# Performance work log

Measured on AMD Instinct MI355X. Metric: run time of the kernel, lower is better.

Reference implementation:

```python
import jax, jax.numpy as jnp
from jax import lax
import numpy as np

B, L, E, K, NCLS = 128, 1024, 8, 3, 5


def conv1d(x, w, b):
    # x: [N,C,L], w: [O,I,3], padding=1 -> same length
    y = lax.conv_general_dilated(x, w, (1,), [(1, 1)], dimension_numbers=('NCH', 'OIH', 'NCH'))
    return y + b[None, :, None]


def maxpool2(x):
    # MaxPool1d(kernel=2, stride=2), floor mode (VALID drops odd tail)
    return lax.reduce_window(x, -jnp.inf, lax.max, (1, 1, 2), (1, 1, 2), 'VALID')


def setup_inputs():
    key = jax.random.key(0)
    ks = jax.random.split(key, 32)
    s = 0.05
    g = lambda i, shp: jax.random.normal(ks[i], shp, jnp.float32) * s
    inp = {}
    inp['x'] = jax.random.normal(ks[0], (B, 1, L), jnp.float32)
    inp['c1_w'], inp['c1_b'] = g(1, (16, 1, 3)), jnp.zeros((16,), jnp.float32)
    # stacked expert conv params (leading dim = E)
    chans = [(16, 16), (16, 32), (32, 64), (64, 128), (128, 256), (256, 512)]
    for j, (ci, co) in enumerate(chans, start=1):
        inp[f'ew{j}'] = g(1 + j, (E, co, ci, 3))
        inp[f'eb{j}'] = jnp.zeros((E, co), jnp.float32)
    inp['r_w'], inp['r_b'] = g(10, (E, 16)), jnp.zeros((E,), jnp.float32)
    inp['c2_w'], inp['c2_b'] = g(11, (1024, 512, 3)), jnp.zeros((1024,), jnp.float32)
    fl = (L // 8 // 2) * 1024
    inp['f1_w'], inp['f1_b'] = g(12, (256, fl)) * 0.2, jnp.zeros((256,), jnp.float32)
    inp['f2_w'], inp['f2_b'] = g(13, (NCLS, 256)), jnp.zeros((NCLS,), jnp.float32)
    return inp


def reference(x, c1_w, c1_b, ew1, eb1, ew2, eb2, ew3, eb3, ew4, eb4, ew5, eb5, ew6, eb6,
              r_w, r_b, c2_w, c2_b, f1_w, f1_b, f2_w, f2_b):
    b = x.shape[0]
    h = jax.nn.relu(conv1d(x, c1_w, c1_b))            # [B,16,L]
    pooled = h.mean(axis=-1)                           # AdaptiveAvgPool1d(1) -> [B,16]
    # (router noise skipped: eval-mode determinism)
    rlogits = pooled @ r_w.T + r_b                     # [B,E]
    probs = jax.nn.softmax(rlogits, axis=-1)
    tg, ti = lax.top_k(probs, K)                       # [B,K]
    tg = tg / tg.sum(axis=-1, keepdims=True)
    gates = jnp.zeros((b, E), probs.dtype).at[jnp.arange(b)[:, None], ti].set(tg)  # dense [B,E]

    def expert(w1, b1, w2, b2, w3, b3, w4, b4, w5, b5, w6, b6):
        y = conv1d(h, w1, b1)
        y = maxpool2(jax.nn.relu(conv1d(y, w2, b2)))   # block1 -> [B,32,L/2]
        y = conv1d(y, w3, b3)
        y = maxpool2(jax.nn.relu(conv1d(y, w4, b4)))   # block2 -> [B,128,L/4]
        y = conv1d(y, w5, b5)
        y = maxpool2(jax.nn.relu(conv1d(y, w6, b6)))   # block3 -> [B,512,L/8]
        return y

    eouts = jax.vmap(expert)(ew1, eb1, ew2, eb2, ew3, eb3, ew4, eb4, ew5, eb5, ew6, eb6)  # [E,B,512,L/8]
    combined = jnp.einsum('be,ebcl->bcl', gates, eouts)  # gated scatter-combine (zero gate == not dispatched)

    y = maxpool2(jax.nn.relu(conv1d(combined, c2_w, c2_b)))  # [B,1024,L/16]
    y = y.reshape(b, -1)
    y = jax.nn.relu(y @ f1_w.T + f1_b)                 # dropout p=0.05 is identity in eval
    out = y @ f2_w.T + f2_b                            # [B,NCLS]

    mean_probs = probs.mean(axis=0)
    cv = jnp.std(mean_probs, ddof=1) / (mean_probs.mean() + 1e-10)  # torch std is unbiased
    return out, cv ** 2
```

## Files before the change

kernel.cpp:

```cpp
#include <hip/hip_runtime.h>
#include <hip/hip_bf16.h>
#include <math.h>

#define B_   128
#define L_   1024
#define E_   8
#define K_   3

typedef float f32x4 __attribute__((ext_vector_type(4)));
typedef short s8v  __attribute__((ext_vector_type(8)));
typedef unsigned short u16x8 __attribute__((ext_vector_type(8)));

__device__ inline ushort f2bf(float v) {
  union { float f; unsigned u; } x; x.f = v;
  unsigned r = (x.u + 0x7fffu + ((x.u >> 16) & 1u)) >> 16;
  return (ushort)r;
}
__device__ inline float bf2f(ushort h) {
  union { unsigned u; float f; } x; x.u = ((unsigned)h) << 16;
  return x.f;
}

__device__ __forceinline__ void gload_lds16(const ushort* g, ushort* l) {
  __builtin_amdgcn_global_load_lds(
      (const __attribute__((address_space(1))) unsigned int*)g,
      (__attribute__((address_space(3))) unsigned int*)l, 16, 0, 0);
}

__global__ __launch_bounds__(256) void conv1_k(
    const float* __restrict__ x, const float* __restrict__ w,
    const float* __restrict__ bias, float* __restrict__ h,
    float* __restrict__ pooled)
{
  const int b = blockIdx.x;
  const int t = threadIdx.x;
  __shared__ float xs[1026];
  __shared__ float wsm[48];
  __shared__ float bs[16];
  __shared__ float red[4][16];

  for (int i = t; i < 1024; i += 256) xs[i + 1] = x[(size_t)b * 1024 + i];
  if (t == 0) { xs[0] = 0.f; xs[1025] = 0.f; }
  if (t < 48) wsm[t] = w[t];
  if (t < 16) bs[t] = bias[t];
  __syncthreads();

  float ps[16];
#pragma unroll
  for (int c = 0; c < 16; ++c) ps[c] = 0.f;

  for (int li = 0; li < 4; ++li) {
    const int l = t + li * 256;
    const float xm = xs[l], x0 = xs[l + 1], xp = xs[l + 2];
#pragma unroll
    for (int co = 0; co < 16; ++co) {
      float v = fmaf(wsm[co * 3 + 0], xm,
                fmaf(wsm[co * 3 + 1], x0,
                fmaf(wsm[co * 3 + 2], xp, bs[co])));
      v = fmaxf(v, 0.f);
      h[((size_t)b * 16 + co) * 1024 + l] = v;
      ps[co] += v;
    }
  }
#pragma unroll
  for (int co = 0; co < 16; ++co) {
    float v = ps[co];
    for (int off = 32; off > 0; off >>= 1) v += __shfl_down(v, off, 64);
    ps[co] = v;
  }
  const int wid = t >> 6, lane = t & 63;
  if (lane == 0) {
#pragma unroll
    for (int co = 0; co < 16; ++co) red[wid][co] = ps[co];
  }
  __syncthreads();
  if (t < 16) pooled[(size_t)b * 16 + t] =
      (red[0][t] + red[1][t] + red[2][t] + red[3][t]) * (1.f / 1024.f);
}

__global__ void router_k(const float* __restrict__ pooled,
                         const float* __restrict__ rw,
                         const float* __restrict__ rb,
                         float* __restrict__ pair_g, int* __restrict__ pair_e,
                         float* __restrict__ cv2_out)
{
  const int b = threadIdx.x;
  __shared__ float pl[128][8];
  __shared__ float mp[8];

  float pv[16];
#pragma unroll
  for (int i = 0; i < 16; ++i) pv[i] = pooled[(size_t)b * 16 + i];

  float lg[8];
#pragma unroll
  for (int e = 0; e < 8; ++e) {
    float s = rb[e];
#pragma unroll
    for (int i = 0; i < 16; ++i) s = fmaf(pv[i], rw[e * 16 + i], s);
    lg[e] = s;
  }
  float mx = lg[0];
#pragma unroll
  for (int e = 1; e < 8; ++e) mx = fmaxf(mx, lg[e]);
  float pr[8]; float sum = 0.f;
#pragma unroll
  for (int e = 0; e < 8; ++e) { pr[e] = expf(lg[e] - mx); sum += pr[e]; }
  const float inv = 1.f / sum;
#pragma unroll
  for (int e = 0; e < 8; ++e) { pr[e] *= inv; pl[b][e] = pr[e]; }

  bool used[8] = {false,false,false,false,false,false,false,false};
  float tg[3]; int ti[3];
  for (int k = 0; k < 3; ++k) {
    float best = -1.f; int bi = 0;
#pragma unroll
    for (int e = 0; e < 8; ++e)
      if (!used[e] && pr[e] > best) { best = pr[e]; bi = e; }
    used[bi] = true; tg[k] = best; ti[k] = bi;
  }
  const float ts = 1.f / (tg[0] + tg[1] + tg[2]);
  for (int k = 0; k < 3; ++k) {
    pair_g[b * 3 + k] = tg[k] * ts;
    pair_e[b * 3 + k] = ti[k];
  }
  __syncthreads();
  if (b < 8) {
    float s = 0.f;
    for (int i = 0; i < 128; ++i) s += pl[i][b];
    mp[b] = s * (1.f / 128.f);
  }
  __syncthreads();
  if (b == 0) {
    float m = 0.f;
    for (int e = 0; e < 8; ++e) m += mp[e];
    m *= (1.f / 8.f);
    float v = 0.f;
    for (int e = 0; e < 8; ++e) { float d = mp[e] - m; v += d * d; }
    v *= (1.f / 7.f);
    const float cv = sqrtf(v) / (m + 1e-10f);
    cv2_out[0] = cv * cv;
  }
}

template <int CI, int CO, int LIN, bool POOL, int CIC, int CO_T, int CO_R,
          int IN_DIV>
__global__ __launch_bounds__(256) void convR_k(
    const float* __restrict__ in, const float* __restrict__ w,
    const float* __restrict__ bias, float* __restrict__ out,
    const int* __restrict__ pe)
{
  constexpr int CQ  = CO_T / CO_R;
  constexpr int LQ  = 256 / CQ;
  constexpr int L_T = LQ * 4;
  constexpr int LOUT = POOL ? (LIN / 2) : LIN;
  constexpr int RS  = L_T + 8;
  constexpr int CG  = CO_R / 4;

  const int p  = blockIdx.x;
  const int cb = blockIdx.y * CO_T;
  const int l0 = blockIdx.z * L_T;
  const int e  = pe ? pe[p] : 0;
  const float* inp = in + (size_t)(p / IN_DIV) * CI * LIN;
  const float* wp  = w + (size_t)e * CO * CI * 3;

  __shared__ float in_s[CIC * RS];
  __shared__ float w_s[CIC * 3 * CO_T];

  const int t  = threadIdx.x;
  const int cq = t / LQ;
  const int lq = t % LQ;

  float acc[CO_R][4];
#pragma unroll
  for (int c = 0; c < CO_R; ++c)
#pragma unroll
    for (int l = 0; l < 4; ++l) acc[c][l] = 0.f;

  for (int c0 = 0; c0 < CI; c0 += CIC) {
    for (int idx = t; idx < CIC * (L_T + 2); idx += 256) {
      const int ci = idx / (L_T + 2);
      const int j  = idx - ci * (L_T + 2);
      const int gl = l0 + j - 1;
      in_s[ci * RS + j] =
          (gl >= 0 && gl < LIN) ? inp[(size_t)(c0 + ci) * LIN + gl] : 0.f;
    }
    for (int i = t; i < CIC * CO_T; i += 256) {
      const int co = i % CO_T;
      const int ci = i / CO_T;
      const float* wsrc = wp + ((size_t)(cb + co) * CI + (c0 + ci)) * 3;
      const float w0 = wsrc[0], w1 = wsrc[1], w2 = wsrc[2];
      w_s[(ci * 3 + 0) * CO_T + co] = w0;
      w_s[(ci * 3 + 1) * CO_T + co] = w1;
      w_s[(ci * 3 + 2) * CO_T + co] = w2;
    }
    __syncthreads();
#pragma unroll 4
    for (int ci = 0; ci < CIC; ++ci) {
      const float* row = &in_s[ci * RS + lq * 4];
      const float4 xa = *reinterpret_cast<const float4*>(row);
      const float2 xb = *reinterpret_cast<const float2*>(row + 4);
      const float xv[6] = {xa.x, xa.y, xa.z, xa.w, xb.x, xb.y};
      const float* wrow = &w_s[ci * 3 * CO_T + cq * CO_R];
#pragma unroll
      for (int k = 0; k < 3; ++k) {
#pragma unroll
        for (int cg = 0; cg < CG; ++cg) {
          const float4 wv =
              *reinterpret_cast<const float4*>(&wrow[k * CO_T + cg * 4]);
          const float wq[4] = {wv.x, wv.y, wv.z, wv.w};
#pragma unroll
          for (int c = 0; c < 4; ++c)
#pragma unroll
            for (int l = 0; l < 4; ++l)
              acc[cg * 4 + c][l] = fmaf(wq[c], xv[l + k], acc[cg * 4 + c][l]);
        }
      }
    }
    __syncthreads();
  }

#pragma unroll
  for (int c = 0; c < CO_R; ++c) {
    const int co = cb + cq * CO_R + c;
    const float bv = bias[(size_t)e * CO + co];
    const float v0 = acc[c][0] + bv, v1 = acc[c][1] + bv;
    const float v2 = acc[c][2] + bv, v3 = acc[c][3] + bv;
    float* op = out + ((size_t)p * CO + co) * LOUT;
    if (POOL) {
      const int lo = (l0 >> 1) + lq * 2;
      float2 r;
      r.x = fmaxf(fmaxf(v0, v1), 0.f);
      r.y = fmaxf(fmaxf(v2, v3), 0.f);
      *reinterpret_cast<float2*>(&op[lo]) = r;
    } else {
      const int l = l0 + lq * 4;
      *reinterpret_cast<float4*>(&op[l]) = make_float4(v0, v1, v2, v3);
    }
  }
}

struct WSeg { const float* w; ushort* oh; ushort* ol; int CO; int CI; int n; };

__global__ void wprepAll_k(const float* w3, const float* w4,
                           const float* w5, const float* w6,
                           const float* wF,
                           ushort* o3h, ushort* o3l, ushort* o4h, ushort* o4l,
                           ushort* o5h, ushort* o5l, ushort* o6h, ushort* o6l,
                           ushort* oFh, ushort* oFl)
{
  int idx = blockIdx.x * 256 + threadIdx.x;
  const float* w; ushort* oh; ushort* ol; int CO, CI;
  if (idx < 49152)        { w = w3; oh = o3h; ol = o3l; CO = 64;   CI = 32;  }
  else if (idx < 245760)  { idx -= 49152;
                            w = w4; oh = o4h; ol = o4l; CO = 128;  CI = 64;  }
  else if (idx < 1032192) { idx -= 245760;
                            w = w5; oh = o5h; ol = o5l; CO = 256;  CI = 128; }
  else if (idx < 4177920) { idx -= 1032192;
                            w = w6; oh = o6h; ol = o6l; CO = 512;  CI = 256; }
  else if (idx < 5750784) { idx -= 4177920;
                            w = wF; oh = oFh; ol = oFl; CO = 1024; CI = 512; }
  else return;

  const int KC = CI >> 5;
  const int j = idx & 31;
  int r = idx >> 5;
  const int co = r % CO; r /= CO;
  const int kc = r % KC; r /= KC;
  const int tp = r % 3;
  const int e  = r / 3;
  const float v = w[(((size_t)e * CO + co) * CI + (kc * 32 + j)) * 3 + tp];
  const ushort hi = f2bf(v);
  oh[idx] = hi;
  ol[idx] = f2bf(v - bf2f(hi));
}

__global__ __launch_bounds__(256) void t0_k(const float* __restrict__ in,
                                            ushort* __restrict__ oh,
                                            ushort* __restrict__ ol)
{
  __shared__ float tile[32][33];
  const int p  = blockIdx.x;
  const int l0 = blockIdx.y * 32;
  const int tx = threadIdx.x & 31;
  const int ty = threadIdx.x >> 5;

#pragma unroll
  for (int i = 0; i < 4; ++i) {
    const int ci = ty + i * 8;
    tile[ci][tx] = in[(size_t)p * 16384 + (size_t)ci * 512 + l0 + tx];
  }
  __syncthreads();
#pragma unroll
  for (int i = 0; i < 4; ++i) {
    const int l = l0 + ty + i * 8;
    const float v = tile[tx][ty + i * 8];
    const size_t o = ((size_t)p * 514 + 1 + l) * 32 + tx;
    const ushort hi = f2bf(v);
    oh[o] = hi;
    ol[o] = f2bf(v - bf2f(hi));
  }
  if (blockIdx.y == 0 && threadIdx.x < 32) {
    const size_t o0 = (size_t)p * 514 * 32 + threadIdx.x;
    const size_t o1 = ((size_t)p * 514 + 513) * 32 + threadIdx.x;
    oh[o0] = 0; ol[o0] = 0; oh[o1] = 0; ol[o1] = 0;
  }
}

template <int CI, int CO, int L, int OMODE>
__global__ __launch_bounds__(256) void convM_k(
    const ushort* __restrict__ xh, const ushort* __restrict__ xl,
    const ushort* __restrict__ wh, const ushort* __restrict__ wl,
    const float* __restrict__ bias,
    ushort* __restrict__ oh, ushort* __restrict__ ol,
    float* __restrict__ of,
    const int* __restrict__ pe, const float* __restrict__ pg,
    int pair0)
{
  constexpr int KC = CI / 32;
  constexpr int NK = (OMODE == 1) ? 3 : 1;
  const int bx = blockIdx.x;
  const int cb = blockIdx.y * 64;
  const int lz = blockIdx.z * 128;

  __shared__ ushort xs[2][130][32];
  __shared__ ushort wsm[2][3][64][32];
  ushort* xsf = &xs[0][0][0];
  ushort* wsf = &wsm[0][0][0][0];

  const int t = threadIdx.x;
  const int lane = t & 63;
  const int wv = t >> 6;
  const int l16 = lane & 15;
  const int kb8 = (lane >> 4) * 8;

  float gacc[2][4][2];
  if (OMODE == 1) {
#pragma unroll
    for (int a = 0; a < 2; ++a)
#pragma unroll
      for (int b = 0; b < 4; ++b) { gacc[a][b][0] = 0.f; gacc[a][b][1] = 0.f; }
  }

  f32x4 acc[2][4];
  int e = 0; float gate = 1.f; int lp = bx;
  float bv[4];

  for (int kp = 0; kp < NK; ++kp) {
    if (OMODE == 1) {
      const int gp = (pair0 + bx) * 3 + kp;
      e = pe[gp]; gate = pg[gp]; lp = bx * 3 + kp;
    } else if (OMODE == 2) { lp = bx; e = 0; }
    else { lp = bx; e = pe[pair0 + bx]; }

#pragma unroll
    for (int a = 0; a < 2; ++a)
#pragma unroll
      for (int b = 0; b < 4; ++b) acc[a][b] = (f32x4){0.f, 0.f, 0.f, 0.f};

    const size_t xbase = ((size_t)lp * (L + 2) + lz) * CI;

    for (int kc = 0; kc < KC; ++kc) {
      const int c0 = kc * 32;
#pragma unroll
      for (int it = 0; it < 5; ++it) {
        const int g = it * 256 + t;
        if (g < 1040) {
          const int pl = g >= 520;
          const int r = g - pl * 520;
          const int row = r >> 2;
          const int c16 = r & 3;
          const ushort* src =
              (pl ? xl : xh) + xbase + (size_t)row * CI + c0 + c16 * 8;
          gload_lds16(src, xsf + (size_t)g * 8);
        }
      }
#pragma unroll
      for (int it = 0; it < 6; ++it) {
        const int g = it * 256 + t;
        const int pl = g >= 768;
        const int r = g - pl * 768;
        const int tp = r >> 8;
        const int rr = r & 255;
        const int co = rr >> 2;
        const int c16 = rr & 3;
        const ushort* src = (pl ? wl : wh) +
            ((((size_t)e * 3 + tp) * KC + kc) * CO + cb + co) * 32 + c16 * 8;
        gload_lds16(src, wsf + (size_t)g * 8);
      }
      __syncthreads();

      __builtin_amdgcn_s_setprio(1);
#pragma unroll
      for (int tp = 0; tp < 3; ++tp) {
        const int ar = wv * 32 + l16 + tp;
        s8v a00 = *reinterpret_cast<const s8v*>(&xs[0][ar][kb8]);
        s8v a01 = *reinterpret_cast<const s8v*>(&xs[0][ar + 16][kb8]);
        s8v a10 = *reinterpret_cast<const s8v*>(&xs[1][ar][kb8]);
        s8v a11 = *reinterpret_cast<const s8v*>(&xs[1][ar + 16][kb8]);
#pragma unroll
        for (int cs = 0; cs < 4; ++cs) {
          const int brow = cs * 16 + l16;
          s8v bh = *reinterpret_cast<const s8v*>(&wsm[0][tp][brow][kb8]);
          s8v bl = *reinterpret_cast<const s8v*>(&wsm[1][tp][brow][kb8]);
          acc[0][cs] = __builtin_amdgcn_mfma_f32_16x16x32_bf16(a00, bh, acc[0][cs], 0, 0, 0);
          acc[0][cs] = __builtin_amdgcn_mfma_f32_16x16x32_bf16(a00, bl, acc[0][cs], 0, 0, 0);
          acc[0][cs] = __builtin_amdgcn_mfma_f32_16x16x32_bf16(a10, bh, acc[0][cs], 0, 0, 0);
          acc[1][cs] = __builtin_amdgcn_mfma_f32_16x16x32_bf16(a01, bh, acc[1][cs], 0, 0, 0);
          acc[1][cs] = __builtin_amdgcn_mfma_f32_16x16x32_bf16(a01, bl, acc[1][cs], 0, 0, 0);
          acc[1][cs] = __builtin_amdgcn_mfma_f32_16x16x32_bf16(a11, bh, acc[1][cs], 0, 0, 0);
        }
      }
      __builtin_amdgcn_s_setprio(0);
      __syncthreads();
    }

#pragma unroll
    for (int cs = 0; cs < 4; ++cs)
      bv[cs] = bias[(size_t)e * CO + cb + cs * 16 + l16];

    if (OMODE == 1) {
#pragma unroll
      for (int ls = 0; ls < 2; ++ls)
#pragma unroll
        for (int cs = 0; cs < 4; ++cs)
#pragma unroll
          for (int q = 0; q < 2; ++q) {
            const float v0 = acc[ls][cs][q * 2] + bv[cs];
            const float v1 = acc[ls][cs][q * 2 + 1] + bv[cs];
            const float m = fmaxf(fmaxf(v0, v1), 0.f);
            gacc[ls][cs][q] += gate * m;
          }
    }
  }

  if (OMODE == 0) {
#pragma unroll
    for (int ls = 0; ls < 2; ++ls)
#pragma unroll
      for (int cs = 0; cs < 4; ++cs)
#pragma unroll
        for (int r = 0; r < 4; ++r) {
          const int l = lz + wv * 32 + ls * 16 + (lane >> 4) * 4 + r;
          const float v = acc[ls][cs][r] + bv[cs];
          const size_t o = ((size_t)lp * (L + 2) + 1 + l) * CO + cb + cs * 16 + l16;
          const ushort hi = f2bf(v);
          oh[o] = hi;
          ol[o] = f2bf(v - bf2f(hi));
        }
    if (blockIdx.z == 0 && t < 64) {
      const size_t o0 = (size_t)lp * (L + 2) * CO + cb + t;
      const size_t o1 = ((size_t)lp * (L + 2) + (L + 1)) * CO + cb + t;
      oh[o0] = 0; ol[o0] = 0; oh[o1] = 0; ol[o1] = 0;
    }
  } else if (OMODE == 3) {
#pragma unroll
    for (int ls = 0; ls < 2; ++ls)
#pragma unroll
      for (int cs = 0; cs < 4; ++cs)
#pragma unroll
        for (int r = 0; r < 4; r += 2) {
          const float v0 = acc[ls][cs][r] + bv[cs];
          const float v1 = acc[ls][cs][r + 1] + bv[cs];
          const float m = fmaxf(fmaxf(v0, v1), 0.f);
          const int lpp = (lz + wv * 32 + ls * 16 + (lane >> 4) * 4 + r) >> 1;
          const size_t o = ((size_t)lp * (L / 2 + 2) + 1 + lpp) * CO + cb + cs * 16 + l16;
          const ushort hi = f2bf(m);
          oh[o] = hi;
          ol[o] = f2bf(m - bf2f(hi));
        }
    if (blockIdx.z == 0 && t < 64) {
      const size_t o0 = (size_t)lp * (L / 2 + 2) * CO + cb + t;
      const size_t o1 = ((size_t)lp * (L / 2 + 2) + (L / 2 + 1)) * CO + cb + t;
      oh[o0] = 0; ol[o0] = 0; oh[o1] = 0; ol[o1] = 0;
    }
  } else if (OMODE == 1) {
#pragma unroll
    for (int ls = 0; ls < 2; ++ls)
#pragma unroll
      for (int cs = 0; cs < 4; ++cs)
#pragma unroll
        for (int q = 0; q < 2; ++q) {
          const int lpp = (lz + wv * 32 + ls * 16 + (lane >> 4) * 4 + q * 2) >> 1;
          const int co = cb + cs * 16 + l16;
          const size_t o =
              ((size_t)(pair0 + bx) * (L / 2 + 2) + 1 + lpp) * CO + co;
          const float g = gacc[ls][cs][q];
          const ushort hi = f2bf(g);
          oh[o] = hi;
          ol[o] = f2bf(g - bf2f(hi));
        }
    if (blockIdx.z == 0 && t < 64) {
      const size_t o0 = (size_t)(pair0 + bx) * (L / 2 + 2) * CO + cb + t;
      const size_t o1 =
          ((size_t)(pair0 + bx) * (L / 2 + 2) + (L / 2 + 1)) * CO + cb + t;
      oh[o0] = 0; ol[o0] = 0; oh[o1] = 0; ol[o1] = 0;
    }
  } else {
#pragma unroll
    for (int ls = 0; ls < 2; ++ls)
#pragma unroll
      for (int cs = 0; cs < 4; ++cs)
#pragma unroll
        for (int r = 0; r < 4; r += 2) {
          const float v0 = acc[ls][cs][r] + bv[cs];
          const float v1 = acc[ls][cs][r + 1] + bv[cs];
          const float m = fmaxf(fmaxf(v0, v1), 0.f);
          const int lpp = (lz + wv * 32 + ls * 16 + (lane >> 4) * 4 + r) >> 1;
          const int co = cb + cs * 16 + l16;
          const size_t o = ((size_t)lp * CO + co) * (L / 2) + lpp;
          of[o] = m;
        }
  }
}

__global__ __launch_bounds__(256) void fc1M_k(const float* __restrict__ X,
                                              const float* __restrict__ W,
                                              float* __restrict__ part)
{
  __shared__ ushort xs[2][128][32];
  __shared__ ushort wsm[2][64][32];
  const int t = threadIdx.x;
  const int lane = t & 63;
  const int wv = t >> 6;
  const int l16 = lane & 15;
  const int kb8 = (lane >> 4) * 8;
  const int ot = blockIdx.x * 64;
  const size_t k0g = (size_t)blockIdx.y * 512;

  f32x4 acc[2][4];
#pragma unroll
  for (int a = 0; a < 2; ++a)
#pragma unroll
    for (int b = 0; b < 4; ++b) acc[a][b] = (f32x4){0.f, 0.f, 0.f, 0.f};

  const int xrow = t >> 1;
  const int xcol = (t & 1) * 16;
  const int wco  = t >> 2;
  const int wk   = (t & 3) * 8;

  for (int it = 0; it < 16; ++it) {
    const size_t k0 = k0g + it * 32;
    {
      const float* src = X + (size_t)xrow * 65536 + k0 + xcol;
      float v[16];
#pragma unroll
      for (int q = 0; q < 4; ++q)
        *reinterpret_cast<float4*>(&v[q * 4]) =
            *reinterpret_cast<const float4*>(src + q * 4);
#pragma unroll
      for (int q = 0; q < 2; ++q) {
        u16x8 hv, lv;
#pragma unroll
        for (int j = 0; j < 8; ++j) {
          const float f = v[q * 8 + j];
          const ushort h = f2bf(f);
          hv[j] = h;
          lv[j] = f2bf(f - bf2f(h));
        }
        *reinterpret_cast<u16x8*>(&xs[0][xrow][xcol + q * 8]) = hv;
        *reinterpret_cast<u16x8*>(&xs[1][xrow][xcol + q * 8]) = lv;
      }
    }
    {
      const float* src = W + (size_t)(ot + wco) * 65536 + k0 + wk;
      float v[8];
      *reinterpret_cast<float4*>(&v[0]) = *reinterpret_cast<const float4*>(src);
      *reinterpret_cast<float4*>(&v[4]) = *reinterpret_cast<const float4*>(src + 4);
      u16x8 hv, lv;
#pragma unroll
      for (int j = 0; j < 8; ++j) {
        const ushort h = f2bf(v[j]);
        hv[j] = h;
        lv[j] = f2bf(v[j] - bf2f(h));
      }
      *reinterpret_cast<u16x8*>(&wsm[0][wco][wk]) = hv;
      *reinterpret_cast<u16x8*>(&wsm[1][wco][wk]) = lv;
    }
    __syncthreads();
    __builtin_amdgcn_s_setprio(1);
#pragma unroll
    for (int ms = 0; ms < 2; ++ms) {
      const int ar = wv * 32 + ms * 16 + l16;
      s8v ah = *reinterpret_cast<const s8v*>(&xs[0][ar][kb8]);
      s8v al = *reinterpret_cast<const s8v*>(&xs[1][ar][kb8]);
#pragma unroll
      for (int cs = 0; cs < 4; ++cs) {
        const int brow = cs * 16 + l16;
        s8v bh = *reinterpret_cast<const s8v*>(&wsm[0][brow][kb8]);
        s8v bl = *reinterpret_cast<const s8v*>(&wsm[1][brow][kb8]);
        acc[ms][cs] = __builtin_amdgcn_mfma_f32_16x16x32_bf16(ah, bh, acc[ms][cs], 0, 0, 0);
        acc[ms][cs] = __builtin_amdgcn_mfma_f32_16x16x32_bf16(ah, bl, acc[ms][cs], 0, 0, 0);
        acc[ms][cs] = __builtin_amdgcn_mfma_f32_16x16x32_bf16(al, bh, acc[ms][cs], 0, 0, 0);
      }
    }
    __builtin_amdgcn_s_setprio(0);
    __syncthreads();
  }

#pragma unroll
  for (int ms = 0; ms < 2; ++ms)
#pragma unroll
    for (int cs = 0; cs < 4; ++cs)
#pragma unroll
      for (int r = 0; r < 4; ++r) {
        const int row = wv * 32 + ms * 16 + (lane >> 4) * 4 + r;
        const int col = ot + cs * 16 + l16;
        part[((size_t)blockIdx.y * 128 + row) * 256 + col] = acc[ms][cs][r];
      }
}

__global__ void fc1red_k(const float* __restrict__ part,
                         const float* __restrict__ b1, float* __restrict__ o1)
{
  const int idx = blockIdx.x * 256 + threadIdx.x;
  if (idx < 32768) {
    float s = 0.f;
#pragma unroll 8
    for (int z = 0; z < 128; ++z) s += part[(size_t)z * 32768 + idx];
    o1[idx] = fmaxf(s + b1[idx & 255], 0.f);
  }
}

__global__ void fc2_k(const float* __restrict__ o1, const float* __restrict__ w2,
                      const float* __restrict__ b2, float* __restrict__ out)
{
  const int b = blockIdx.x;
  const int lane = threadIdx.x;
  float acc[5] = {0.f, 0.f, 0.f, 0.f, 0.f};
  for (int i = lane; i < 256; i += 64) {
    const float xv = o1[(size_t)b * 256 + i];
#pragma unroll
    for (int o = 0; o < 5; ++o) acc[o] = fmaf(xv, w2[o * 256 + i], acc[o]);
  }
#pragma unroll
  for (int o = 0; o < 5; ++o) {
    for (int off = 32; off > 0; off >>= 1)
      acc[o] += __shfl_down(acc[o], off, 64);
  }
  if (lane == 0) {
#pragma unroll
    for (int o = 0; o < 5; ++o) out[b * 5 + o] = acc[o] + b2[o];
  }
}

extern "C" void kernel_launch(void* const* d_in, const int* in_sizes, int n_in,
                              void* d_out, int out_size, void* d_ws,
                              size_t ws_size, hipStream_t stream)
{
  const float* x   = (const float*)d_in[0];
  const float* c1w = (const float*)d_in[1];
  const float* c1b = (const float*)d_in[2];
  const float* ew[6];
  const float* eb[6];
  for (int j = 0; j < 6; ++j) {
    ew[j] = (const float*)d_in[3 + 2 * j];
    eb[j] = (const float*)d_in[4 + 2 * j];
  }
  const float* rw  = (const float*)d_in[15];
  const float* rb  = (const float*)d_in[16];
  const float* c2w = (const float*)d_in[17];
  const float* c2b = (const float*)d_in[18];
  const float* f1w = (const float*)d_in[19];
  const float* f1b = (const float*)d_in[20];
  const float* f2w = (const float*)d_in[21];
  const float* f2b = (const float*)d_in[22];
  float* out = (float*)d_out;

  const int chunkB = 32;
  const int chunkP = chunkB * 3;
  const int nchunk = 128 / chunkB;

  char* basep = (char*)d_ws;
  size_t off = 0;
  auto alloc = [&](size_t bytes) -> void* {
    off = (off + 255) & ~(size_t)255;
    void* r = basep + off;
    off += bytes;
    return r;
  };

  float* h      = (float*)alloc(2097152ull * 4);
  float* pooled = (float*)alloc(2048ull * 4);
  float* pairg  = (float*)alloc(384ull * 4);
  int*   paire  = (int*)  alloc(384ull * 4);
  float* fc1o   = (float*)alloc(32768ull * 4);

  ushort* xtFh  = (ushort*)alloc(8519680ull * 2 * 2);
  ushort* xtFl  = xtFh + 8519680ull;
  float*  part  = (float*)xtFh;

  const size_t slot_base = (off + 255) & ~(size_t)255;
  char* slotA = (char*)alloc((size_t)chunkP * 33024 * 2 * 2);
  char* slotB = (char*)alloc((size_t)chunkP * 66048 * 2 * 2);
  float* comb = (float*)(basep + slot_base);

  float*  bufA  = (float*)slotA;
  ushort* xt3h  = (ushort*)slotA;
  ushort* xt3l  = xt3h + (size_t)chunkP * 16448;
  ushort* xt5h  = (ushort*)slotA;
  ushort* xt5l  = xt5h + (size_t)chunkP * 33024;
  float*  bufB  = (float*)slotB;
  ushort* yE3h  = (ushort*)slotB;
  ushort* yE3l  = yE3h + (size_t)chunkP * 32896;
  ushort* y5h   = (ushort*)slotB;
  ushort* y5l   = y5h + (size_t)chunkP * 66048;

  ushort* wp3h  = (ushort*)alloc(49152ull * 2);
  ushort* wp3l  = (ushort*)alloc(49152ull * 2);
  ushort* wp4h  = (ushort*)alloc(196608ull * 2);
  ushort* wp4l  = (ushort*)alloc(196608ull * 2);
  ushort* wp5h  = (ushort*)alloc(786432ull * 2);
  ushort* wp5l  = (ushort*)alloc(786432ull * 2);
  ushort* wp6h  = (ushort*)alloc(3145728ull * 2);
  ushort* wp6l  = (ushort*)alloc(3145728ull * 2);
  ushort* wpFh  = (ushort*)alloc(1572864ull * 2);
  ushort* wpFl  = (ushort*)alloc(1572864ull * 2);

  conv1_k<<<128, 256, 0, stream>>>(x, c1w, c1b, h, pooled);
  router_k<<<1, 128, 0, stream>>>(pooled, rw, rb, pairg, paire, out + 640);

  wprepAll_k<<<(5750784 + 255) / 256, 256, 0, stream>>>(
      ew[2], ew[3], ew[4], ew[5], c2w,
      wp3h, wp3l, wp4h, wp4l, wp5h, wp5l, wp6h, wp6l, wpFh, wpFl);

  for (int c = 0; c < nchunk; ++c) {
    const int b0 = c * chunkB;
    const int p0 = c * chunkP;
    convR_k<16, 16, 1024, false, 16, 16, 4, 3>
        <<<dim3(chunkP, 1, 4), 256, 0, stream>>>(
            h + (size_t)b0 * 16 * 1024, ew[0], eb[0], bufA, paire + p0);
    convR_k<16, 32, 1024, true, 16, 32, 8, 1>
        <<<dim3(chunkP, 1, 4), 256, 0, stream>>>(bufA, ew[1], eb[1], bufB,
                                                 paire + p0);
    t0_k<<<dim3(chunkP, 16), 256, 0, stream>>>(bufB, xt3h, xt3l);
    convM_k<32, 64, 512, 0>
        <<<dim3(chunkP, 1, 4), 256, 0, stream>>>(xt3h, xt3l, wp3h, wp3l, eb[2],
                                                 yE3h, yE3l, nullptr, paire,
                                                 nullptr, p0);
    convM_k<64, 128, 512, 3>
        <<<dim3(chunkP, 2, 4), 256, 0, stream>>>(yE3h, yE3l, wp4h, wp4l, eb[3],
                                                 xt5h, xt5l, nullptr, paire,
                                                 nullptr, p0);
    convM_k<128, 256, 256, 0>
        <<<dim3(chunkP, 4, 2), 256, 0, stream>>>(xt5h, xt5l, wp5h, wp5l, eb[4],
                                                 y5h, y5l, nullptr, paire,
                                                 nullptr, p0);
    convM_k<256, 512, 256, 1>
        <<<dim3(chunkB, 8, 2), 256, 0, stream>>>(y5h, y5l, wp6h, wp6l, eb[5],
                                                 xtFh, xtFl, nullptr,
                                                 paire, pairg, b0);
  }

  convM_k<512, 1024, 128, 2>
      <<<dim3(128, 16, 1), 256, 0, stream>>>(xtFh, xtFl, wpFh, wpFl, c2b,
                                             nullptr, nullptr, comb, nullptr,
                                             nullptr, 0);

  fc1M_k<<<dim3(4, 128), 256, 0, stream>>>(comb, f1w, part);
  fc1red_k<<<128, 256, 0, stream>>>(part, f1b, fc1o);
  fc2_k<<<128, 64, 0, stream>>>(fc1o, f2w, f2b, out);
}
```

Baseline: 643.2 us.

## Fuse transpose/bf16 split into conv2 epilogue and enlarge batch chunk

The second expert conv kernel now writes its pooled output directly in the transposed, padded bf16 hi/lo layout that the MFMA conv consumes, which removes the separate t0_k transpose kernel and its fp32 round trip through memory. The xt3 buffer gets its own allocation because it can no longer alias slotA. The batch chunk size also grows to 64 when the workspace is large enough, halving the number of per-chunk launches at the cost of more workspace. The fused stores are strided scalar ushort writes (stride CO), which may coalesce worse than the old tiled transpose.

```diff
diff --git a/kernel.cpp b/kernel.cpp
--- a/kernel.cpp
+++ b/kernel.cpp
@@ -144,10 +144,11 @@
 }
 
 template <int CI, int CO, int LIN, bool POOL, int CIC, int CO_T, int CO_R,
-          int IN_DIV>
+          int IN_DIV, bool TPOSE>
 __global__ __launch_bounds__(256) void convR_k(
     const float* __restrict__ in, const float* __restrict__ w,
     const float* __restrict__ bias, float* __restrict__ out,
+    ushort* __restrict__ oh, ushort* __restrict__ ol,
     const int* __restrict__ pe)
 {
   constexpr int CQ  = CO_T / CO_R;
@@ -226,21 +227,39 @@
     const float bv = bias[(size_t)e * CO + co];
     const float v0 = acc[c][0] + bv, v1 = acc[c][1] + bv;
     const float v2 = acc[c][2] + bv, v3 = acc[c][3] + bv;
-    float* op = out + ((size_t)p * CO + co) * LOUT;
-    if (POOL) {
+    if (TPOSE) {
+      const float m0 = fmaxf(fmaxf(v0, v1), 0.f);
+      const float m1 = fmaxf(fmaxf(v2, v3), 0.f);
       const int lo = (l0 >> 1) + lq * 2;
-      float2 r;
-      r.x = fmaxf(fmaxf(v0, v1), 0.f);
-      r.y = fmaxf(fmaxf(v2, v3), 0.f);
-      *reinterpret_cast<float2*>(&op[lo]) = r;
+      const size_t o0 = ((size_t)p * (LIN / 2 + 2) + 1 + lo) * CO + co;
+      const ushort h0 = f2bf(m0);
+      oh[o0] = h0;
+      ol[o0] = f2bf(m0 - bf2f(h0));
+      const ushort h1 = f2bf(m1);
+      oh[o0 + CO] = h1;
+      ol[o0 + CO] = f2bf(m1 - bf2f(h1));
     } else {
-      const int l = l0 + lq * 4;
-      *reinterpret_cast<float4*>(&op[l]) = make_float4(v0, v1, v2, v3);
-    }
-  }
-}
-
-struct WSeg { const float* w; ushort* oh; ushort* ol; int CO; int CI; int n; };
+      float* op = out + ((size_t)p * CO + co) * LOUT;
+      if (POOL) {
+        const int lo = (l0 >> 1) + lq * 2;
+        float2 r;
+        r.x = fmaxf(fmaxf(v0, v1), 0.f);
+        r.y = fmaxf(fmaxf(v2, v3), 0.f);
+        *reinterpret_cast<float2*>(&op[lo]) = r;
+      } else {
+        const int l = l0 + lq * 4;
+        *reinterpret_cast<float4*>(&op[l]) = make_float4(v0, v1, v2, v3);
+      }
+    }
+  }
+  if (TPOSE) {
+    if (blockIdx.z == 0 && t < CO) {
+      const size_t o0 = (size_t)p * (LIN / 2 + 2) * CO + t;
+      const size_t o1 = ((size_t)p * (LIN / 2 + 2) + (LIN / 2 + 1)) * CO + t;
+      oh[o0] = 0; ol[o0] = 0; oh[o1] = 0; ol[o1] = 0;
+    }
+  }
+}
 
 __global__ void wprepAll_k(const float* w3, const float* w4,
                            const float* w5, const float* w6,
@@ -273,38 +292,6 @@
   const ushort hi = f2bf(v);
   oh[idx] = hi;
   ol[idx] = f2bf(v - bf2f(hi));
-}
-
-__global__ __launch_bounds__(256) void t0_k(const float* __restrict__ in,
-                                            ushort* __restrict__ oh,
-                                            ushort* __restrict__ ol)
-{
-  __shared__ float tile[32][33];
-  const int p  = blockIdx.x;
-  const int l0 = blockIdx.y * 32;
-  const int tx = threadIdx.x & 31;
-  const int ty = threadIdx.x >> 5;
-
-#pragma unroll
-  for (int i = 0; i < 4; ++i) {
-    const int ci = ty + i * 8;
-    tile[ci][tx] = in[(size_t)p * 16384 + (size_t)ci * 512 + l0 + tx];
-  }
-  __syncthreads();
-#pragma unroll
-  for (int i = 0; i < 4; ++i) {
-    const int l = l0 + ty + i * 8;
-    const float v = tile[tx][ty + i * 8];
-    const size_t o = ((size_t)p * 514 + 1 + l) * 32 + tx;
-    const ushort hi = f2bf(v);
-    oh[o] = hi;
-    ol[o] = f2bf(v - bf2f(hi));
-  }
-  if (blockIdx.y == 0 && threadIdx.x < 32) {
-    const size_t o0 = (size_t)p * 514 * 32 + threadIdx.x;
-    const size_t o1 = ((size_t)p * 514 + 513) * 32 + threadIdx.x;
-    oh[o0] = 0; ol[o0] = 0; oh[o1] = 0; ol[o1] = 0;
-  }
 }
 
 template <int CI, int CO, int L, int OMODE>
@@ -667,7 +654,7 @@
   const float* f2b = (const float*)d_in[22];
   float* out = (float*)d_out;
 
-  const int chunkB = 32;
+  const int chunkB = (ws_size >= 160000000ull) ? 64 : 32;
   const int chunkP = chunkB * 3;
   const int nchunk = 128 / chunkB;
 
@@ -691,20 +678,20 @@
   float*  part  = (float*)xtFh;
 
   const size_t slot_base = (off + 255) & ~(size_t)255;
-  char* slotA = (char*)alloc((size_t)chunkP * 33024 * 2 * 2);
-  char* slotB = (char*)alloc((size_t)chunkP * 66048 * 2 * 2);
+  char* slotA = (char*)alloc((size_t)chunkP * 132096);
+  char* slotB = (char*)alloc((size_t)chunkP * 264192);
   float* comb = (float*)(basep + slot_base);
 
   float*  bufA  = (float*)slotA;
-  ushort* xt3h  = (ushort*)slotA;
-  ushort* xt3l  = xt3h + (size_t)chunkP * 16448;
   ushort* xt5h  = (ushort*)slotA;
   ushort* xt5l  = xt5h + (size_t)chunkP * 33024;
-  float*  bufB  = (float*)slotB;
   ushort* yE3h  = (ushort*)slotB;
   ushort* yE3l  = yE3h + (size_t)chunkP * 32896;
   ushort* y5h   = (ushort*)slotB;
   ushort* y5l   = y5h + (size_t)chunkP * 66048;
+
+  ushort* xt3h  = (ushort*)alloc((size_t)chunkP * 16448 * 2 * 2);
+  ushort* xt3l  = xt3h + (size_t)chunkP * 16448;
 
   ushort* wp3h  = (ushort*)alloc(49152ull * 2);
   ushort* wp3l  = (ushort*)alloc(49152ull * 2);
@@ -727,13 +714,13 @@
   for (int c = 0; c < nchunk; ++c) {
     const int b0 = c * chunkB;
     const int p0 = c * chunkP;
-    convR_k<16, 16, 1024, false, 16, 16, 4, 3>
+    convR_k<16, 16, 1024, false, 16, 16, 4, 3, false>
         <<<dim3(chunkP, 1, 4), 256, 0, stream>>>(
-            h + (size_t)b0 * 16 * 1024, ew[0], eb[0], bufA, paire + p0);
-    convR_k<16, 32, 1024, true, 16, 32, 8, 1>
-        <<<dim3(chunkP, 1, 4), 256, 0, stream>>>(bufA, ew[1], eb[1], bufB,
-                                                 paire + p0);
-    t0_k<<<dim3(chunkP, 16), 256, 0, stream>>>(bufB, xt3h, xt3l);
+            h + (size_t)b0 * 16 * 1024, ew[0], eb[0], bufA, nullptr, nullptr,
+            paire + p0);
+    convR_k<16, 32, 1024, true, 16, 32, 8, 1, true>
+        <<<dim3(chunkP, 1, 4), 256, 0, stream>>>(bufA, ew[1], eb[1], nullptr,
+                                                 xt3h, xt3l, paire + p0);
     convM_k<32, 64, 512, 0>
         <<<dim3(chunkP, 1, 4), 256, 0, stream>>>(xt3h, xt3l, wp3h, wp3l, eb[2],
                                                  yE3h, yE3l, nullptr, paire,
```

Measured after the change: 567.7 us. 1.13x faster.
